# Optimization experiments

Hardware: AMD Instinct MI355X
Metric: run time of the kernel (lower is better)

Reference implementation:

```python
import jax, jax.numpy as jnp
import numpy as np

N_NODES = 100000
N_EDGES = 1600000
NUM_GRAPHS = 2000
IN_CH, HID = 5, 64
NEG_SLOPE = 0.2


def _lin_params(key, out_d, in_d, bias=True):
    k1, k2 = jax.random.split(key)
    bound = 1.0 / np.sqrt(in_d)
    W = jax.random.uniform(k1, (out_d, in_d), jnp.float32, -bound, bound)
    if bias:
        b = jax.random.uniform(k2, (out_d,), jnp.float32, -bound, bound)
        return W, b
    return (W,)


def setup_inputs() -> dict:
    key = jax.random.key(0)
    ks = jax.random.split(key, 12)
    x = jax.random.normal(ks[0], (N_NODES, IN_CH), jnp.float32)
    edge_index = jax.random.randint(ks[1], (2, N_EDGES), 0, N_NODES, jnp.int64)
    batch = (jnp.arange(N_NODES, dtype=jnp.int64) * NUM_GRAPHS) // N_NODES  # 50 nodes/graph, sorted
    # SAGEConv params: lin_l (on aggregated neighbors, with bias), lin_r (root, no bias)
    W1l, b1 = _lin_params(ks[2], HID, IN_CH)
    (W1r,) = _lin_params(ks[3], HID, IN_CH, bias=False)
    W2l, b2 = _lin_params(ks[4], 2 * HID, HID)
    (W2r,) = _lin_params(ks[5], 2 * HID, HID, bias=False)
    W3l, b3 = _lin_params(ks[6], 4 * HID, 2 * HID)
    (W3r,) = _lin_params(ks[7], 4 * HID, 2 * HID, bias=False)
    # classifier MLP: 512 -> 128 -> 64 -> 1
    Wc1, bc1 = _lin_params(ks[8], 2 * HID, 8 * HID)
    Wc2, bc2 = _lin_params(ks[9], HID, 2 * HID)
    Wc3, bc3 = _lin_params(ks[10], 1, HID)
    return {
        "x": x, "edge_index": edge_index, "batch": batch, "num_graphs": NUM_GRAPHS,
        "W1l": W1l, "b1": b1, "W1r": W1r,
        "W2l": W2l, "b2": b2, "W2r": W2r,
        "W3l": W3l, "b3": b3, "W3r": W3r,
        "Wc1": Wc1, "bc1": bc1, "Wc2": Wc2, "bc2": bc2, "Wc3": Wc3, "bc3": bc3,
    }


def _sage_conv(x, src, dst, Wl, b, Wr):
    # mean-aggregate messages x[src] at dst, then lin_l(agg) + lin_r(x)
    n = x.shape[0]
    s = jax.ops.segment_sum(x[src], dst, num_segments=n)
    cnt = jax.ops.segment_sum(jnp.ones((src.shape[0],), x.dtype), dst, num_segments=n)
    mean = s / jnp.maximum(cnt, 1.0)[:, None]
    return mean @ Wl.T + b + x @ Wr.T


def reference(x, edge_index, batch, num_graphs,
              W1l, b1, W1r, W2l, b2, W2r, W3l, b3, W3r,
              Wc1, bc1, Wc2, bc2, Wc3, bc3):
    src, dst = edge_index[0], edge_index[1]
    lrelu = lambda h: jax.nn.leaky_relu(h, NEG_SLOPE)
    h = lrelu(_sage_conv(x, src, dst, W1l, b1, W1r))
    h = lrelu(_sage_conv(h, src, dst, W2l, b2, W2r))
    h = lrelu(_sage_conv(h, src, dst, W3l, b3, W3r))
    # global mean + max pool per graph -> [G, 512]
    s = jax.ops.segment_sum(h, batch, num_segments=num_graphs)
    cnt = jax.ops.segment_sum(jnp.ones((h.shape[0],), h.dtype), batch, num_segments=num_graphs)
    mean_p = s / jnp.maximum(cnt, 1.0)[:, None]
    max_p = jax.ops.segment_max(h, batch, num_segments=num_graphs)
    g = jnp.concatenate([mean_p, max_p], axis=1)
    # classifier (dropout = identity in eval mode)
    g = lrelu(g @ Wc1.T + bc1)
    g = lrelu(g @ Wc2.T + bc2)
    logits = g @ Wc3.T + bc3
    return logits.squeeze(-1)
```

## Files before the change

kernel.cpp:

```cpp
#include <hip/hip_runtime.h>
#include <cstdint>
#include <cstddef>

#define NEG_SLOPE 0.2f

typedef __attribute__((ext_vector_type(8))) short bh8;
typedef __attribute__((ext_vector_type(16))) float f32x16;

__device__ inline void splitf(float x, short& hi, short& lo) {
    uint32_t u = __float_as_uint(x);
    uint32_t rh = (u + 0x7FFFu + ((u >> 16) & 1u)) & 0xFFFF0000u;
    hi = (short)(rh >> 16);
    float rem = x - __uint_as_float(rh);
    uint32_t u2 = __float_as_uint(rem);
    lo = (short)((u2 + 0x7FFFu + ((u2 >> 16) & 1u)) >> 16);
}

__global__ void sentinel_kernel(float* __restrict__ out, int n) {
    int i = blockIdx.x * blockDim.x + threadIdx.x;
    if (i < n) out[i] = 12345.0f;
}

#define HIST_CH 8192
__global__ void bucket_count_kernel(const int* __restrict__ dst, int* __restrict__ bcnt,
                                    int ne, int nb) {
    __shared__ int hist[256];
    const int tid = threadIdx.x;
    hist[tid] = 0;
    __syncthreads();
    int e0 = blockIdx.x * HIST_CH;
    for (int i = tid; i < HIST_CH; i += 256) {
        int e = e0 + i;
        if (e < ne) atomicAdd(&hist[dst[e] >> 9], 1);
    }
    __syncthreads();
    if (tid < nb && hist[tid] > 0) atomicAdd(&bcnt[tid], hist[tid]);
}

__global__ void scan256_kernel(const int* __restrict__ bcnt, int* __restrict__ boff, int n) {
    const int tid = threadIdx.x, lane = tid & 63, wid = tid >> 6;
    __shared__ int wt[4];
    int v = (tid < n) ? bcnt[tid] : 0;
    int incl = v;
    #pragma unroll
    for (int o = 1; o < 64; o <<= 1) {
        int t = __shfl_up(incl, o);
        if (lane >= o) incl += t;
    }
    if (lane == 63) wt[wid] = incl;
    __syncthreads();
    if (tid < 4) {
        int w = wt[tid], winc = w;
        #pragma unroll
        for (int o = 1; o < 4; o <<= 1) {
            int t = __shfl_up(winc, o);
            if (tid >= o) winc += t;
        }
        wt[tid] = winc - w;
    }
    __syncthreads();
    int excl = wt[wid] + incl - v;
    if (tid < n) boff[tid] = excl;
    if (tid == n - 1) boff[n] = excl + v;
}

#define SCAT_CH 4096
__global__ void bucket_scatter_kernel(const int* __restrict__ src, const int* __restrict__ dst,
                                      const int* __restrict__ boff, int* __restrict__ bcur,
                                      unsigned* __restrict__ pairs, int ne, int nb) {
    __shared__ int hist[256], lcur[256], gbase[256];
    const int tid = threadIdx.x;
    hist[tid] = 0; lcur[tid] = 0;
    __syncthreads();
    int e0 = blockIdx.x * SCAT_CH;
    for (int i = tid; i < SCAT_CH; i += 256) {
        int e = e0 + i;
        if (e < ne) atomicAdd(&hist[dst[e] >> 9], 1);
    }
    __syncthreads();
    if (tid < nb) {
        int h = hist[tid];
        gbase[tid] = (h > 0) ? (boff[tid] + atomicAdd(&bcur[tid], h)) : 0;
    }
    __syncthreads();
    for (int i = tid; i < SCAT_CH; i += 256) {
        int e = e0 + i;
        if (e < ne) {
            int d = dst[e];
            int b = d >> 9;
            int r = atomicAdd(&lcur[b], 1);
            pairs[gbase[b] + r] = ((unsigned)(d & 511) << 17) | (unsigned)src[e];
        }
    }
}

__global__ __launch_bounds__(512) void bucket_sort_kernel(
        const unsigned* __restrict__ pairs, const int* __restrict__ boff,
        int* __restrict__ off, int* __restrict__ csr, int n_nodes) {
    __shared__ int cnt[512], lcur[512];
    __shared__ int wt[8];
    const int b = blockIdx.x;
    const int tid = threadIdx.x, lane = tid & 63, wid = tid >> 6;
    const int s = boff[b], t = boff[b + 1];
    cnt[tid] = 0; lcur[tid] = 0;
    __syncthreads();
    for (int i = s + tid; i < t; i += 512)
        atomicAdd(&cnt[pairs[i] >> 17], 1);
    __syncthreads();
    int v = cnt[tid];
    int incl = v;
    #pragma unroll
    for (int o = 1; o < 64; o <<= 1) {
        int tt = __shfl_up(incl, o);
        if (lane >= o) incl += tt;
    }
    if (lane == 63) wt[wid] = incl;
    __syncthreads();
    if (tid < 8) {
        int w = wt[tid], winc = w;
        #pragma unroll
        for (int o = 1; o < 8; o <<= 1) {
            int tt = __shfl_up(winc, o);
            if (tid >= o) winc += tt;
        }
        wt[tid] = winc - w;
    }
    __syncthreads();
    int excl = wt[wid] + incl - v;
    __syncthreads();
    cnt[tid] = excl;
    int node = b * 512 + tid;
    if (node < n_nodes) off[node] = s + excl;
    if (b == 0 && tid == 0) off[n_nodes] = boff[gridDim.x];
    __syncthreads();
    for (int i = s + tid; i < t; i += 512) {
        unsigned p = pairs[i];
        int bin = p >> 17;
        int r = atomicAdd(&lcur[bin], 1);
        csr[s + cnt[bin] + r] = (int)(p & 0x1FFFFu);
    }
}

__global__ void pack_wsplit_kernel(const float* __restrict__ Wl, const float* __restrict__ Wr,
                                   short* __restrict__ Whi, short* __restrict__ Wlo,
                                   int COUT, int K, int CIN) {
    int i = blockIdx.x * blockDim.x + threadIdx.x;
    if (i >= COUT * K) return;
    int n = i / K, k = i % K;
    float v = (k < CIN) ? Wl[n * CIN + k] : Wr[n * CIN + (k - CIN)];
    short h, l;
    splitf(v, h, l);
    Whi[i] = h; Wlo[i] = l;
}

__global__ __launch_bounds__(256) void sage1_kernel(
        const float* __restrict__ x, const int* __restrict__ off,
        const int* __restrict__ csr, const float* __restrict__ W1l,
        const float* __restrict__ W1r, const float* __restrict__ b1,
        float* __restrict__ h1, int n_nodes) {
    __shared__ float sWl[320], sWr[320], sb[64];
    const int tid = threadIdx.x;
    for (int i = tid; i < 320; i += 256) { sWl[i] = W1l[i]; sWr[i] = W1r[i]; }
    if (tid < 64) sb[tid] = b1[tid];
    __syncthreads();
    int node = blockIdx.x * 4 + (tid >> 6);
    int lane = tid & 63;
    if (node >= n_nodes) return;
    int slot = lane >> 3, cg = lane & 7;
    int e0 = off[node], cnt = off[node + 1] - e0;
    float a0 = 0.f, a1 = 0.f;
    int i = slot;
    for (; i + 8 < cnt; i += 16) {
        int s0 = csr[e0 + i];
        int s1 = csr[e0 + i + 8];
        a0 += (cg < 5) ? x[(size_t)s0 * 5 + cg] : 0.f;
        a1 += (cg < 5) ? x[(size_t)s1 * 5 + cg] : 0.f;
    }
    for (; i < cnt; i += 8) {
        int s = csr[e0 + i];
        a0 += (cg < 5) ? x[(size_t)s * 5 + cg] : 0.f;
    }
    float acc = a0 + a1;
    #pragma unroll
    for (int o = 8; o < 64; o <<= 1) acc += __shfl_xor(acc, o);
    float inv = (cnt > 0) ? 1.f / (float)cnt : 0.f;
    float m = acc * inv;
    float xv = (lane < 5) ? x[(size_t)node * 5 + lane] : 0.f;
    float o = sb[lane];
    #pragma unroll
    for (int c = 0; c < 5; ++c) {
        o += sWl[lane * 5 + c] * __shfl(m, c);
        o += sWr[lane * 5 + c] * __shfl(xv, c);
    }
    o = o > 0.f ? o : o * NEG_SLOPE;
    h1[(size_t)node * 64 + lane] = o;
}

template<int CIN>
__global__ void agg_vec3_kernel(const float* __restrict__ h, const int* __restrict__ off,
                                const int* __restrict__ csr, float* __restrict__ mean,
                                int n_nodes) {
    constexpr int HALVES = CIN / 64;
    int wid = blockIdx.x * (blockDim.x >> 6) + (threadIdx.x >> 6);
    int lane = threadIdx.x & 63;
    if (wid >= n_nodes * HALVES) return;
    int node = (HALVES == 1) ? wid : (wid >> 1);
    int half = (HALVES == 1) ? 0 : (wid & 1);
    int slot = lane >> 4, cg = lane & 15;
    int e0 = off[node], cnt = off[node + 1] - e0;
    const float* hb = h + (size_t)half * 64 + cg * 4;
    float4 a0 = {0.f,0.f,0.f,0.f}, a1 = {0.f,0.f,0.f,0.f};
    float4 a2 = {0.f,0.f,0.f,0.f}, a3 = {0.f,0.f,0.f,0.f};
    int i = slot;
    for (; i + 12 < cnt; i += 16) {
        int s0 = csr[e0 + i];
        int s1 = csr[e0 + i + 4];
        int s2 = csr[e0 + i + 8];
        int s3 = csr[e0 + i + 12];
        float4 v0 = *(const float4*)(hb + (size_t)s0 * CIN);
        float4 v1 = *(const float4*)(hb + (size_t)s1 * CIN);
        float4 v2 = *(const float4*)(hb + (size_t)s2 * CIN);
        float4 v3 = *(const float4*)(hb + (size_t)s3 * CIN);
        a0.x += v0.x; a0.y += v0.y; a0.z += v0.z; a0.w += v0.w;
        a1.x += v1.x; a1.y += v1.y; a1.z += v1.z; a1.w += v1.w;
        a2.x += v2.x; a2.y += v2.y; a2.z += v2.z; a2.w += v2.w;
        a3.x += v3.x; a3.y += v3.y; a3.z += v3.z; a3.w += v3.w;
    }
    for (; i < cnt; i += 4) {
        int s = csr[e0 + i];
        float4 v = *(const float4*)(hb + (size_t)s * CIN);
        a0.x += v.x; a0.y += v.y; a0.z += v.z; a0.w += v.w;
    }
    float4 acc;
    acc.x = (a0.x + a1.x) + (a2.x + a3.x);
    acc.y = (a0.y + a1.y) + (a2.y + a3.y);
    acc.z = (a0.z + a1.z) + (a2.z + a3.z);
    acc.w = (a0.w + a1.w) + (a2.w + a3.w);
    #pragma unroll
    for (int o = 16; o < 64; o <<= 1) {
        acc.x += __shfl_xor(acc.x, o);
        acc.y += __shfl_xor(acc.y, o);
        acc.z += __shfl_xor(acc.z, o);
        acc.w += __shfl_xor(acc.w, o);
    }
    if (slot == 0) {
        float inv = (cnt > 0) ? 1.f / (float)cnt : 0.f;
        float4 r = {acc.x * inv, acc.y * inv, acc.z * inv, acc.w * inv};
        *(float4*)(mean + (size_t)node * CIN + half * 64 + cg * 4) = r;
    }
}

#define BM 128
#define BN 64
#define BK 16

template<bool RELU>
__global__ __launch_bounds__(256) void gemm_cat_kernel(
        const float* __restrict__ AL, const float* __restrict__ AR,
        const float* __restrict__ W, const float* __restrict__ bias,
        float* __restrict__ C, int M, int N, int K, int CIN) {
    __shared__ float As[BK][BM + 4];
    __shared__ float Bs[BK][BN + 4];
    const int row0 = blockIdx.x * BM;
    const int col0 = blockIdx.y * BN;
    const int tid = threadIdx.x;
    const int ttm = tid & 15, ttn = tid >> 4;

    float acc[8][4];
    #pragma unroll
    for (int i = 0; i < 8; ++i)
        #pragma unroll
        for (int j = 0; j < 4; ++j) acc[i][j] = 0.f;

    for (int k0 = 0; k0 < K; k0 += BK) {
        for (int i = tid; i < BM * BK; i += 256) {
            int m = i >> 4, k = i & 15;
            int r = row0 + m, kk = k0 + k;
            float v = 0.f;
            if (r < M && kk < K)
                v = (kk < CIN) ? AL[(size_t)r * CIN + kk]
                               : AR[(size_t)r * CIN + (kk - CIN)];
            As[k][m] = v;
        }
        for (int i = tid; i < BN * BK; i += 256) {
            int n = i >> 4, k = i & 15;
            int c = col0 + n, kk = k0 + k;
            Bs[k][n] = (c < N && kk < K) ? W[(size_t)c * K + kk] : 0.f;
        }
        __syncthreads();
        #pragma unroll
        for (int k = 0; k < BK; ++k) {
            float4 a0 = *(const float4*)&As[k][ttm * 8];
            float4 a1 = *(const float4*)&As[k][ttm * 8 + 4];
            float4 b0 = *(const float4*)&Bs[k][ttn * 4];
            float av[8] = {a0.x, a0.y, a0.z, a0.w, a1.x, a1.y, a1.z, a1.w};
            float bv[4] = {b0.x, b0.y, b0.z, b0.w};
            #pragma unroll
            for (int i = 0; i < 8; ++i)
                #pragma unroll
                for (int j = 0; j < 4; ++j)
                    acc[i][j] += av[i] * bv[j];
        }
        __syncthreads();
    }

    float bv[4];
    #pragma unroll
    for (int j = 0; j < 4; ++j) bv[j] = bias[col0 + ttn * 4 + j];
    #pragma unroll
    for (int i = 0; i < 8; ++i) {
        int r = row0 + ttm * 8 + i;
        if (r < M) {
            float t0 = acc[i][0] + bv[0];
            float t1 = acc[i][1] + bv[1];
            float t2 = acc[i][2] + bv[2];
            float t3 = acc[i][3] + bv[3];
            if (RELU) {
                t0 = t0 > 0.f ? t0 : t0 * NEG_SLOPE;
                t1 = t1 > 0.f ? t1 : t1 * NEG_SLOPE;
                t2 = t2 > 0.f ? t2 : t2 * NEG_SLOPE;
                t3 = t3 > 0.f ? t3 : t3 * NEG_SLOPE;
            }
            float4 v; v.x = t0; v.y = t1; v.z = t2; v.w = t3;
            *(float4*)&C[(size_t)r * N + col0 + ttn * 4] = v;
        }
    }
}

__global__ __launch_bounds__(256) void gemm_cat_mfma_kernel(
        const float* __restrict__ AL, const float* __restrict__ AR,
        const short* __restrict__ Whi, const short* __restrict__ Wlo,
        const float* __restrict__ bias, float* __restrict__ C,
        int M, int N, int K, int CIN) {
    __shared__ short AsH[128][40], AsL[128][40];
    __shared__ short BsH[128][40], BsL[128][40];
    const int row0 = blockIdx.x * 128;
    const int n0 = blockIdx.y * 128;
    const int tid = threadIdx.x;
    const int w = tid >> 6;
    const int lane31 = tid & 31, lhalf = (tid & 63) >> 5;

    f32x16 acc[4];
    #pragma unroll
    for (int ci = 0; ci < 4; ++ci)
        #pragma unroll
        for (int r = 0; r < 16; ++r) acc[ci][r] = 0.f;

    for (int k0 = 0; k0 < K; k0 += 32) {
        const float* Asrc = (k0 < CIN) ? AL : AR;
        const int kb = (k0 < CIN) ? k0 : k0 - CIN;
        {
            int row = tid >> 1, kq = (tid & 1) * 16;
            int r = row0 + row;
            float vv[16];
            #pragma unroll
            for (int i = 0; i < 16; ++i) vv[i] = 0.f;
            if (r < M) {
                const float* p = &Asrc[(size_t)r * CIN + kb + kq];
                #pragma unroll
                for (int q = 0; q < 4; ++q) {
                    float4 v = ((const float4*)p)[q];
                    vv[q * 4 + 0] = v.x; vv[q * 4 + 1] = v.y;
                    vv[q * 4 + 2] = v.z; vv[q * 4 + 3] = v.w;
                }
            }
            #pragma unroll
            for (int half = 0; half < 2; ++half) {
                bh8 h8, l8;
                #pragma unroll
                for (int i = 0; i < 8; ++i) {
                    short a, b;
                    splitf(vv[half * 8 + i], a, b);
                    h8[i] = a; l8[i] = b;
                }
                *(bh8*)&AsH[row][kq + half * 8] = h8;
                *(bh8*)&AsL[row][kq + half * 8] = l8;
            }
        }
        {
            int n = tid & 127, half = tid >> 7;
            const short* src = half ? Wlo : Whi;
            const uint4* p = (const uint4*)&src[(size_t)(n0 + n) * K + k0];
            if (half) {
                #pragma unroll
                for (int q = 0; q < 4; ++q) *(uint4*)&BsL[n][q * 8] = p[q];
            } else {
                #pragma unroll
                for (int q = 0; q < 4; ++q) *(uint4*)&BsH[n][q * 8] = p[q];
            }
        }
        __syncthreads();
        #pragma unroll
        for (int ks = 0; ks < 2; ++ks) {
            int kofs = ks * 16 + lhalf * 8;
            bh8 aH = *(bh8*)&AsH[w * 32 + lane31][kofs];
            bh8 aL = *(bh8*)&AsL[w * 32 + lane31][kofs];
            #pragma unroll
            for (int ci = 0; ci < 4; ++ci) {
                bh8 bH = *(bh8*)&BsH[ci * 32 + lane31][kofs];
                bh8 bL = *(bh8*)&BsL[ci * 32 + lane31][kofs];
                acc[ci] = __builtin_amdgcn_mfma_f32_32x32x16_bf16(aH, bH, acc[ci], 0, 0, 0);
                acc[ci] = __builtin_amdgcn_mfma_f32_32x32x16_bf16(aH, bL, acc[ci], 0, 0, 0);
                acc[ci] = __builtin_amdgcn_mfma_f32_32x32x16_bf16(aL, bH, acc[ci], 0, 0, 0);
            }
        }
        __syncthreads();
    }

    #pragma unroll
    for (int ci = 0; ci < 4; ++ci) {
        int col = n0 + ci * 32 + lane31;
        float b = bias[col];
        #pragma unroll
        for (int r = 0; r < 16; ++r) {
            int row = row0 + w * 32 + (r & 3) + 8 * (r >> 2) + 4 * lhalf;
            if (row < M) {
                float v = acc[ci][r] + b;
                v = v > 0.f ? v : v * NEG_SLOPE;
                C[(size_t)row * N + col] = v;
            }
        }
    }
}

__global__ __launch_bounds__(512) void gemm_pool_mfma2_kernel(
        const float* __restrict__ AL, const float* __restrict__ AR,
        const short* __restrict__ Whi, const short* __restrict__ Wlo,
        const float* __restrict__ bias, float* __restrict__ gout,
        int npg, int CIN, int NCH) {
    __shared__ short AsH[128][40], AsL[128][40];
    __shared__ short BsH[256][40], BsL[256][40];
    __shared__ float redS[4][258], redM[4][258];
    const int g2 = blockIdx.x * 2;
    const int K = 2 * CIN;
    const int tid = threadIdx.x;
    const int w = tid >> 6;
    const int lane31 = tid & 31, lhalf = (tid & 63) >> 5;
    const int rt = w & 3, cb = (w >> 2) * 4;

    f32x16 acc[4];
    #pragma unroll
    for (int ci = 0; ci < 4; ++ci)
        #pragma unroll
        for (int r = 0; r < 16; ++r) acc[ci][r] = 0.f;

    for (int k0 = 0; k0 < K; k0 += 32) {
        const float* Asrc = (k0 < CIN) ? AL : AR;
        const int kb = (k0 < CIN) ? k0 : k0 - CIN;
        {
            int row = tid >> 2, kq = (tid & 3) * 8;
            int grow = row >> 6, r = row & 63;
            float vv[8];
            #pragma unroll
            for (int i = 0; i < 8; ++i) vv[i] = 0.f;
            if (r < npg) {
                const float* p = &Asrc[((size_t)(g2 + grow) * npg + r) * CIN + kb + kq];
                #pragma unroll
                for (int q = 0; q < 2; ++q) {
                    float4 v = ((const float4*)p)[q];
                    vv[q * 4 + 0] = v.x; vv[q * 4 + 1] = v.y;
                    vv[q * 4 + 2] = v.z; vv[q * 4 + 3] = v.w;
                }
            }
            bh8 h8, l8;
            #pragma unroll
            for (int i = 0; i < 8; ++i) {
                short a, b;
                splitf(vv[i], a, b);
                h8[i] = a; l8[i] = b;
            }
            *(bh8*)&AsH[row][kq] = h8;
            *(bh8*)&AsL[row][kq] = l8;
        }
        {
            int n = tid & 255, half = tid >> 8;
            const short* srcw = half ? Wlo : Whi;
            const uint4* p = (const uint4*)&srcw[(size_t)n * K + k0];
            if (half) {
                #pragma unroll
                for (int q = 0; q < 4; ++q) *(uint4*)&BsL[n][q * 8] = p[q];
            } else {
                #pragma unroll
                for (int q = 0; q < 4; ++q) *(uint4*)&BsH[n][q * 8] = p[q];
            }
        }
        __syncthreads();
        #pragma unroll
        for (int ks = 0; ks < 2; ++ks) {
            int kofs = ks * 16 + lhalf * 8;
            bh8 aH = *(bh8*)&AsH[rt * 32 + lane31][kofs];
            bh8 aL = *(bh8*)&AsL[rt * 32 + lane31][kofs];
            #pragma unroll
            for (int ci = 0; ci < 4; ++ci) {
                bh8 bH = *(bh8*)&BsH[(cb + ci) * 32 + lane31][kofs];
                bh8 bL = *(bh8*)&BsL[(cb + ci) * 32 + lane31][kofs];
                acc[ci] = __builtin_amdgcn_mfma_f32_32x32x16_bf16(aH, bH, acc[ci], 0, 0, 0);
                acc[ci] = __builtin_amdgcn_mfma_f32_32x32x16_bf16(aH, bL, acc[ci], 0, 0, 0);
                acc[ci] = __builtin_amdgcn_mfma_f32_32x32x16_bf16(aL, bH, acc[ci], 0, 0, 0);
            }
        }
        __syncthreads();
    }

    #pragma unroll
    for (int ci = 0; ci < 4; ++ci) {
        int col = (cb + ci) * 32 + lane31;
        float b = bias[col];
        float ls = 0.f, lm = -__builtin_huge_valf();
        #pragma unroll
        for (int r = 0; r < 16; ++r) {
            int crow = (r & 3) + 8 * (r >> 2) + 4 * lhalf;
            int grow = (rt & 1) * 32 + crow;
            if (grow < npg) {
                float v = acc[ci][r] + b;
                v = v > 0.f ? v : v * NEG_SLOPE;
                ls += v;
                lm = fmaxf(lm, v);
            }
        }
        ls += __shfl_xor(ls, 32);
        lm = fmaxf(lm, __shfl_xor(lm, 32));
        if (lhalf == 0) { redS[rt][col] = ls; redM[rt][col] = lm; }
    }
    __syncthreads();
    {
        int c = tid & 255, gi = tid >> 8;
        float s = redS[gi * 2][c] + redS[gi * 2 + 1][c];
        float m = fmaxf(redM[gi * 2][c], redM[gi * 2 + 1][c]);
        gout[(size_t)(g2 + gi) * (2 * NCH) + c] = s / (float)npg;
        gout[(size_t)(g2 + gi) * (2 * NCH) + NCH + c] = m;
    }
}

__global__ void final_kernel(const float* __restrict__ c2, const float* __restrict__ Wc3,
                             const float* __restrict__ bc3, float* __restrict__ out, int G) {
    int g = blockIdx.x * (blockDim.x >> 6) + (threadIdx.x >> 6);
    int lane = threadIdx.x & 63;
    if (g >= G) return;
    float v = c2[(size_t)g * 64 + lane] * Wc3[lane];
    #pragma unroll
    for (int o = 32; o > 0; o >>= 1) v += __shfl_down(v, o);
    if (lane == 0) out[g] = v + bc3[0];
}

extern "C" void kernel_launch(void* const* d_in, const int* in_sizes, int n_in,
                              void* d_out, int out_size, void* d_ws, size_t ws_size,
                              hipStream_t stream) {
    const float* x   = (const float*)d_in[0];
    const int* ei    = (const int*)d_in[1];
    const float* W1l = (const float*)d_in[4];
    const float* b1  = (const float*)d_in[5];
    const float* W1r = (const float*)d_in[6];
    const float* W2l = (const float*)d_in[7];
    const float* b2  = (const float*)d_in[8];
    const float* W2r = (const float*)d_in[9];
    const float* W3l = (const float*)d_in[10];
    const float* b3  = (const float*)d_in[11];
    const float* W3r = (const float*)d_in[12];
    const float* Wc1 = (const float*)d_in[13];
    const float* bc1 = (const float*)d_in[14];
    const float* Wc2 = (const float*)d_in[15];
    const float* bc2 = (const float*)d_in[16];
    const float* Wc3 = (const float*)d_in[17];
    const float* bc3 = (const float*)d_in[18];
    float* out = (float*)d_out;

    const int nodes = in_sizes[0] / 5;
    const int ne    = in_sizes[1] / 2;
    const int G     = out_size;
    const int npg   = nodes / G;
    const int nb    = (nodes + 511) >> 9;

    char* ws = (char*)d_ws;
    size_t pos = 0;
    auto take = [&](size_t bytes) -> char* {
        char* p = ws + pos;
        pos += (bytes + 255) & ~(size_t)255;
        return p;
    };
    int* off     = (int*)take((size_t)(nodes + 1) * 4);
    int* csr     = (int*)take((size_t)ne * 4);
    int* bcnt    = (int*)take(256 * 4);
    int* boff    = (int*)take(257 * 4);
    int* bcur    = (int*)take(256 * 4);
    short* Whi2  = (short*)take((size_t)128 * 128 * 2);
    short* Wlo2  = (short*)take((size_t)128 * 128 * 2);
    short* Whi3  = (short*)take((size_t)256 * 256 * 2);
    short* Wlo3  = (short*)take((size_t)256 * 256 * 2);
    short* WhiC  = (short*)take((size_t)128 * 512 * 2);
    short* WloC  = (short*)take((size_t)128 * 512 * 2);
    float* gbuf  = (float*)take((size_t)G * 512 * 4);
    float* c1    = (float*)take((size_t)G * 128 * 4);
    float* c2    = (float*)take((size_t)G * 64 * 4);
    float* mean1 = (float*)take((size_t)nodes * 64 * 4);
    float* h1    = (float*)take((size_t)nodes * 64 * 4);
    float* h2    = (float*)take((size_t)nodes * 128 * 4);
    float* mean2 = mean1;
    unsigned* pairs = (unsigned*)mean1;

    if (pos > ws_size) {
        sentinel_kernel<<<(G + 255) / 256, 256, 0, stream>>>(out, G);
        return;
    }

    const int* src = ei;
    const int* dst = ei + ne;

    hipMemsetAsync(bcnt, 0, 256 * 4, stream);
    hipMemsetAsync(bcur, 0, 256 * 4, stream);

    bucket_count_kernel<<<(ne + HIST_CH - 1) / HIST_CH, 256, 0, stream>>>(dst, bcnt, ne, nb);
    scan256_kernel<<<1, 256, 0, stream>>>(bcnt, boff, nb);
    bucket_scatter_kernel<<<(ne + SCAT_CH - 1) / SCAT_CH, 256, 0, stream>>>(
        src, dst, boff, bcur, pairs, ne, nb);
    bucket_sort_kernel<<<nb, 512, 0, stream>>>(pairs, boff, off, csr, nodes);

    pack_wsplit_kernel<<<(128 * 128 + 255) / 256, 256, 0, stream>>>(W2l, W2r, Whi2, Wlo2, 128, 128, 64);
    pack_wsplit_kernel<<<(256 * 256 + 255) / 256, 256, 0, stream>>>(W3l, W3r, Whi3, Wlo3, 256, 256, 128);
    pack_wsplit_kernel<<<(128 * 512 + 255) / 256, 256, 0, stream>>>(Wc1, Wc1, WhiC, WloC, 128, 512, 512);

    sage1_kernel<<<(nodes + 3) / 4, 256, 0, stream>>>(x, off, csr, W1l, W1r, b1, h1, nodes);

    agg_vec3_kernel<64><<<(nodes + 3) / 4, 256, 0, stream>>>(h1, off, csr, mean1, nodes);
    {
        dim3 g((nodes + 127) / 128, 1);
        gemm_cat_mfma_kernel<<<g, 256, 0, stream>>>(mean1, h1, Whi2, Wlo2, b2, h2,
                                                    nodes, 128, 128, 64);
    }
    agg_vec3_kernel<128><<<(nodes * 2 + 3) / 4, 256, 0, stream>>>(h2, off, csr, mean2, nodes);
    gemm_pool_mfma2_kernel<<<G / 2, 512, 0, stream>>>(mean2, h2, Whi3, Wlo3, b3, gbuf,
                                                      npg, 128, 256);
    {
        dim3 g((G + 127) / 128, 1);
        gemm_cat_mfma_kernel<<<g, 256, 0, stream>>>(gbuf, gbuf, WhiC, WloC, bc1, c1,
                                                    G, 128, 512, 512);
    }
    {
        dim3 g((G + BM - 1) / BM, 64 / BN);
        gemm_cat_kernel<true><<<g, 256, 0, stream>>>(c1, nullptr, Wc2, bc2, c2, G, 64, 128, 128);
    }
    final_kernel<<<(G + 3) / 4, 256, 0, stream>>>(c2, Wc3, bc3, out, G);
}
```

Before: 467.8 us.

## Gather neighbor features from bf16 shadow copies in mean aggregation

The sage1 and layer-2 GEMM kernels now also write a bf16 copy of their fp32 outputs. The aggregation kernels gather 16-byte bf16 rows from these copies and accumulate in fp32, which halves the bytes moved in the random-access gathers. Layer 2 also uses one wave per node instead of two half-waves. The cost is extra bf16 writes and a drop in precision of the aggregated means, which the hi/lo split GEMMs were built to preserve. The two bucket memsets are merged into one by making the buffers adjacent.

After: 407.1 us. 13.0% less time.

```diff
diff --git a/kernel.cpp b/kernel.cpp
--- a/kernel.cpp
+++ b/kernel.cpp
@@ -14,6 +14,11 @@
     float rem = x - __uint_as_float(rh);
     uint32_t u2 = __float_as_uint(rem);
     lo = (short)((u2 + 0x7FFFu + ((u2 >> 16) & 1u)) >> 16);
+}
+
+__device__ inline unsigned short f2bf(float x) {
+    uint32_t u = __float_as_uint(x);
+    return (unsigned short)((u + 0x7FFFu + ((u >> 16) & 1u)) >> 16);
 }
 
 __global__ void sentinel_kernel(float* __restrict__ out, int n) {
@@ -157,7 +162,7 @@
         const float* __restrict__ x, const int* __restrict__ off,
         const int* __restrict__ csr, const float* __restrict__ W1l,
         const float* __restrict__ W1r, const float* __restrict__ b1,
-        float* __restrict__ h1, int n_nodes) {
+        float* __restrict__ h1, unsigned short* __restrict__ h1b, int n_nodes) {
     __shared__ float sWl[320], sWr[320], sb[64];
     const int tid = threadIdx.x;
     for (int i = tid; i < 320; i += 256) { sWl[i] = W1l[i]; sWr[i] = W1r[i]; }
@@ -194,59 +199,80 @@
     }
     o = o > 0.f ? o : o * NEG_SLOPE;
     h1[(size_t)node * 64 + lane] = o;
+    h1b[(size_t)node * 64 + lane] = f2bf(o);
 }
 
 template<int CIN>
-__global__ void agg_vec3_kernel(const float* __restrict__ h, const int* __restrict__ off,
-                                const int* __restrict__ csr, float* __restrict__ mean,
-                                int n_nodes) {
-    constexpr int HALVES = CIN / 64;
-    int wid = blockIdx.x * (blockDim.x >> 6) + (threadIdx.x >> 6);
+__global__ void agg_bf16_kernel(const unsigned short* __restrict__ hb,
+                                const int* __restrict__ off, const int* __restrict__ csr,
+                                float* __restrict__ mean, int n_nodes) {
+    constexpr int LPR = CIN / 8;
+    constexpr int SLOTS = 64 / LPR;
+    constexpr int UN = 16 / SLOTS;
+    int node = blockIdx.x * (blockDim.x >> 6) + (threadIdx.x >> 6);
     int lane = threadIdx.x & 63;
-    if (wid >= n_nodes * HALVES) return;
-    int node = (HALVES == 1) ? wid : (wid >> 1);
-    int half = (HALVES == 1) ? 0 : (wid & 1);
-    int slot = lane >> 4, cg = lane & 15;
+    if (node >= n_nodes) return;
+    int slot = lane / LPR, cg = lane % LPR;
     int e0 = off[node], cnt = off[node + 1] - e0;
-    const float* hb = h + (size_t)half * 64 + cg * 4;
-    float4 a0 = {0.f,0.f,0.f,0.f}, a1 = {0.f,0.f,0.f,0.f};
-    float4 a2 = {0.f,0.f,0.f,0.f}, a3 = {0.f,0.f,0.f,0.f};
+    const unsigned short* base = hb + cg * 8;
+    float acc[UN][8];
+    #pragma unroll
+    for (int u = 0; u < UN; ++u)
+        #pragma unroll
+        for (int k = 0; k < 8; ++k) acc[u][k] = 0.f;
     int i = slot;
-    for (; i + 12 < cnt; i += 16) {
-        int s0 = csr[e0 + i];
-        int s1 = csr[e0 + i + 4];
-        int s2 = csr[e0 + i + 8];
-        int s3 = csr[e0 + i + 12];
-        float4 v0 = *(const float4*)(hb + (size_t)s0 * CIN);
-        float4 v1 = *(const float4*)(hb + (size_t)s1 * CIN);
-        float4 v2 = *(const float4*)(hb + (size_t)s2 * CIN);
-        float4 v3 = *(const float4*)(hb + (size_t)s3 * CIN);
-        a0.x += v0.x; a0.y += v0.y; a0.z += v0.z; a0.w += v0.w;
-        a1.x += v1.x; a1.y += v1.y; a1.z += v1.z; a1.w += v1.w;
-        a2.x += v2.x; a2.y += v2.y; a2.z += v2.z; a2.w += v2.w;
-        a3.x += v3.x; a3.y += v3.y; a3.z += v3.z; a3.w += v3.w;
-    }
-    for (; i < cnt; i += 4) {
-        int s = csr[e0 + i];
-        float4 v = *(const float4*)(hb + (size_t)s * CIN);
-        a0.x += v.x; a0.y += v.y; a0.z += v.z; a0.w += v.w;
-    }
-    float4 acc;
-    acc.x = (a0.x + a1.x) + (a2.x + a3.x);
-    acc.y = (a0.y + a1.y) + (a2.y + a3.y);
-    acc.z = (a0.z + a1.z) + (a2.z + a3.z);
-    acc.w = (a0.w + a1.w) + (a2.w + a3.w);
-    #pragma unroll
-    for (int o = 16; o < 64; o <<= 1) {
-        acc.x += __shfl_xor(acc.x, o);
-        acc.y += __shfl_xor(acc.y, o);
-        acc.z += __shfl_xor(acc.z, o);
-        acc.w += __shfl_xor(acc.w, o);
-    }
+    for (; i + (UN - 1) * SLOTS < cnt; i += UN * SLOTS) {
+        int s[UN];
+        #pragma unroll
+        for (int u = 0; u < UN; ++u) s[u] = csr[e0 + i + u * SLOTS];
+        uint4 v[UN];
+        #pragma unroll
+        for (int u = 0; u < UN; ++u)
+            v[u] = *(const uint4*)(base + (size_t)s[u] * CIN);
+        #pragma unroll
+        for (int u = 0; u < UN; ++u) {
+            unsigned w0 = v[u].x, w1 = v[u].y, w2 = v[u].z, w3 = v[u].w;
+            acc[u][0] += __uint_as_float(w0 << 16);
+            acc[u][1] += __uint_as_float(w0 & 0xFFFF0000u);
+            acc[u][2] += __uint_as_float(w1 << 16);
+            acc[u][3] += __uint_as_float(w1 & 0xFFFF0000u);
+            acc[u][4] += __uint_as_float(w2 << 16);
+            acc[u][5] += __uint_as_float(w2 & 0xFFFF0000u);
+            acc[u][6] += __uint_as_float(w3 << 16);
+            acc[u][7] += __uint_as_float(w3 & 0xFFFF0000u);
+        }
+    }
+    for (; i < cnt; i += SLOTS) {
+        uint4 v = *(const uint4*)(base + (size_t)csr[e0 + i] * CIN);
+        unsigned w0 = v.x, w1 = v.y, w2 = v.z, w3 = v.w;
+        acc[0][0] += __uint_as_float(w0 << 16);
+        acc[0][1] += __uint_as_float(w0 & 0xFFFF0000u);
+        acc[0][2] += __uint_as_float(w1 << 16);
+        acc[0][3] += __uint_as_float(w1 & 0xFFFF0000u);
+        acc[0][4] += __uint_as_float(w2 << 16);
+        acc[0][5] += __uint_as_float(w2 & 0xFFFF0000u);
+        acc[0][6] += __uint_as_float(w3 << 16);
+        acc[0][7] += __uint_as_float(w3 & 0xFFFF0000u);
+    }
+    float r[8];
+    #pragma unroll
+    for (int k = 0; k < 8; ++k) {
+        float s = acc[0][k];
+        #pragma unroll
+        for (int u = 1; u < UN; ++u) s += acc[u][k];
+        r[k] = s;
+    }
+    #pragma unroll
+    for (int o = LPR; o < 64; o <<= 1)
+        #pragma unroll
+        for (int k = 0; k < 8; ++k) r[k] += __shfl_xor(r[k], o);
     if (slot == 0) {
         float inv = (cnt > 0) ? 1.f / (float)cnt : 0.f;
-        float4 r = {acc.x * inv, acc.y * inv, acc.z * inv, acc.w * inv};
-        *(float4*)(mean + (size_t)node * CIN + half * 64 + cg * 4) = r;
+        float4 lo = {r[0] * inv, r[1] * inv, r[2] * inv, r[3] * inv};
+        float4 hi = {r[4] * inv, r[5] * inv, r[6] * inv, r[7] * inv};
+        float* mp = mean + (size_t)node * CIN + cg * 8;
+        *(float4*)mp = lo;
+        *(float4*)(mp + 4) = hi;
     }
 }
 
@@ -331,6 +357,7 @@
         const float* __restrict__ AL, const float* __restrict__ AR,
         const short* __restrict__ Whi, const short* __restrict__ Wlo,
         const float* __restrict__ bias, float* __restrict__ C,
+        unsigned short* __restrict__ Cb16,
         int M, int N, int K, int CIN) {
     __shared__ short AsH[128][40], AsL[128][40];
     __shared__ short BsH[128][40], BsL[128][40];
@@ -418,6 +445,7 @@
                 float v = acc[ci][r] + b;
                 v = v > 0.f ? v : v * NEG_SLOPE;
                 C[(size_t)row * N + col] = v;
+                if (Cb16) Cb16[(size_t)row * N + col] = f2bf(v);
             }
         }
     }
@@ -581,8 +609,8 @@
     int* off     = (int*)take((size_t)(nodes + 1) * 4);
     int* csr     = (int*)take((size_t)ne * 4);
     int* bcnt    = (int*)take(256 * 4);
+    int* bcur    = (int*)take(256 * 4);
     int* boff    = (int*)take(257 * 4);
-    int* bcur    = (int*)take(256 * 4);
     short* Whi2  = (short*)take((size_t)128 * 128 * 2);
     short* Wlo2  = (short*)take((size_t)128 * 128 * 2);
     short* Whi3  = (short*)take((size_t)256 * 256 * 2);
@@ -595,6 +623,9 @@
     float* mean1 = (float*)take((size_t)nodes * 64 * 4);
     float* h1    = (float*)take((size_t)nodes * 64 * 4);
     float* h2    = (float*)take((size_t)nodes * 128 * 4);
+    char* R      = take((size_t)nodes * 128 * 2);
+    unsigned short* h1b = (unsigned short*)R;
+    unsigned short* h2b = (unsigned short*)R;
     float* mean2 = mean1;
     unsigned* pairs = (unsigned*)mean1;
 
@@ -606,8 +637,7 @@
     const int* src = ei;
     const int* dst = ei + ne;
 
-    hipMemsetAsync(bcnt, 0, 256 * 4, stream);
-    hipMemsetAsync(bcur, 0, 256 * 4, stream);
+    hipMemsetAsync(bcnt, 0, 512 * 4, stream);
 
     bucket_count_kernel<<<(ne + HIST_CH - 1) / HIST_CH, 256, 0, stream>>>(dst, bcnt, ne, nb);
     scan256_kernel<<<1, 256, 0, stream>>>(bcnt, boff, nb);
@@ -619,20 +649,20 @@
     pack_wsplit_kernel<<<(256 * 256 + 255) / 256, 256, 0, stream>>>(W3l, W3r, Whi3, Wlo3, 256, 256, 128);
     pack_wsplit_kernel<<<(128 * 512 + 255) / 256, 256, 0, stream>>>(Wc1, Wc1, WhiC, WloC, 128, 512, 512);
 
-    sage1_kernel<<<(nodes + 3) / 4, 256, 0, stream>>>(x, off, csr, W1l, W1r, b1, h1, nodes);
-
-    agg_vec3_kernel<64><<<(nodes + 3) / 4, 256, 0, stream>>>(h1, off, csr, mean1, nodes);
+    sage1_kernel<<<(nodes + 3) / 4, 256, 0, stream>>>(x, off, csr, W1l, W1r, b1, h1, h1b, nodes);
+
+    agg_bf16_kernel<64><<<(nodes + 3) / 4, 256, 0, stream>>>(h1b, off, csr, mean1, nodes);
     {
         dim3 g((nodes + 127) / 128, 1);
-        gemm_cat_mfma_kernel<<<g, 256, 0, stream>>>(mean1, h1, Whi2, Wlo2, b2, h2,
+        gemm_cat_mfma_kernel<<<g, 256, 0, stream>>>(mean1, h1, Whi2, Wlo2, b2, h2, h2b,
                                                     nodes, 128, 128, 64);
     }
-    agg_vec3_kernel<128><<<(nodes * 2 + 3) / 4, 256, 0, stream>>>(h2, off, csr, mean2, nodes);
+    agg_bf16_kernel<128><<<(nodes + 3) / 4, 256, 0, stream>>>(h2b, off, csr, mean2, nodes);
     gemm_pool_mfma2_kernel<<<G / 2, 512, 0, stream>>>(mean2, h2, Whi3, Wlo3, b3, gbuf,
                                                       npg, 128, 256);
     {
         dim3 g((G + 127) / 128, 1);
-        gemm_cat_mfma_kernel<<<g, 256, 0, stream>>>(gbuf, gbuf, WhiC, WloC, bc1, c1,
+        gemm_cat_mfma_kernel<<<g, 256, 0, stream>>>(gbuf, gbuf, WhiC, WloC, bc1, c1, nullptr,
                                                     G, 128, 512, 512);
     }
     {
```
